# Kernel optimization log

Measured on AMD Instinct MI355X. Metric: run time of the kernel, lower is better.

## Reference

```python
import jax, jax.numpy as jnp
import numpy as np

NC = 80          # classes
REG_MAX = 16     # DFL bins
NK = 51          # 17*3 keypoint channels
KPT_SHAPE = (17, 3)
MAX_DET = 100
CONF_THRES = 0.25
STRIDES = (8, 16, 32)


def _conv1x1(f, w, b):
    # f: (B,C,H,W), w: (O,C), b: (O,) -> (B,O,H,W)
    return jnp.einsum('bchw,oc->bohw', f, w) + b[None, :, None, None]


def _make_anchors(shapes, strides, offset=0.5):
    pts, sts = [], []
    for (h, w), s in zip(shapes, strides):
        sx = jnp.arange(w, dtype=jnp.float32) + offset
        sy = jnp.arange(h, dtype=jnp.float32) + offset
        gy, gx = jnp.meshgrid(sy, sx, indexing='ij')
        pts.append(jnp.stack([gx, gy], -1).reshape(-1, 2))
        sts.append(jnp.full((h * w, 1), float(s), jnp.float32))
    # transposed as in _new_inference: anchors (2,A), strides (1,A)
    return jnp.concatenate(pts, 0).T, jnp.concatenate(sts, 0).T


def setup_inputs() -> dict:
    key = jax.random.key(0)
    ks = jax.random.split(key, 16)
    ch = (128, 256, 512)
    hw = ((80, 80), (40, 40), (20, 20))
    d = {}
    for i, (c, (h, w)) in enumerate(zip(ch, hw)):
        d[f'x{i}'] = jax.random.normal(ks[i], (16, c, h, w), jnp.float32)
    k = 3
    for name, oc in (('cv2', 4 * REG_MAX), ('cv3', NC), ('cv4', NK)):
        for i, c in enumerate(ch):
            d[f'{name}_w{i}'] = jax.random.normal(ks[k], (oc, c), jnp.float32) * 0.02
            d[f'{name}_b{i}'] = jnp.zeros((oc,), jnp.float32)
            k += 1
    return d


def reference(x0, x1, x2,
              cv2_w0, cv2_b0, cv2_w1, cv2_b1, cv2_w2, cv2_b2,
              cv3_w0, cv3_b0, cv3_w1, cv3_b1, cv3_w2, cv3_b2,
              cv4_w0, cv4_b0, cv4_w1, cv4_b1, cv4_w2, cv4_b2):
    feats = [x0, x1, x2]
    cv2 = [(cv2_w0, cv2_b0), (cv2_w1, cv2_b1), (cv2_w2, cv2_b2)]
    cv3 = [(cv3_w0, cv3_b0), (cv3_w1, cv3_b1), (cv3_w2, cv3_b2)]
    cv4 = [(cv4_w0, cv4_b0), (cv4_w1, cv4_b1), (cv4_w2, cv4_b2)]
    bs = x0.shape[0]

    # keypoint branch: cat over levels -> (bs, nk, A)
    kpt = jnp.concatenate(
        [_conv1x1(f, w, b).reshape(bs, NK, -1) for f, (w, b) in zip(feats, cv4)], -1)
    # box+cls branch -> (bs, 4*reg_max+nc, A)
    xcat = jnp.concatenate(
        [jnp.concatenate([_conv1x1(f, *cv2[i]), _conv1x1(f, *cv3[i])], 1).reshape(bs, 4 * REG_MAX + NC, -1)
         for i, f in enumerate(feats)], -1)
    box, cls = xcat[:, :4 * REG_MAX], xcat[:, 4 * REG_MAX:]

    shapes = [(f.shape[2], f.shape[3]) for f in feats]
    anchors, strides = _make_anchors(shapes, STRIDES)  # (2,A), (1,A)
    A = anchors.shape[1]

    # DFL decode: softmax over reg_max bins, expectation w/ arange weights
    p = jax.nn.softmax(box.reshape(bs, 4, REG_MAX, A), axis=2)
    dist = jnp.einsum('bfra,r->bfa', p, jnp.arange(REG_MAX, dtype=jnp.float32))
    lt, rb = dist[:, :2], dist[:, 2:]
    x1y1 = anchors[None] - lt
    x2y2 = anchors[None] + rb
    # xywh box coding, scaled by strides
    dbox = jnp.concatenate([(x1y1 + x2y2) * 0.5, x2y2 - x1y1], 1) * strides[None]  # (bs,4,A)

    # keypoint decode (Pose.kpts_decode, ndim==3)
    y = kpt.reshape(bs, KPT_SHAPE[0], KPT_SHAPE[1], A)
    kxy = (y[:, :, :2] * 2.0 + (anchors[None, None] - 0.5)) * strides[None, None]
    kv = jax.nn.sigmoid(y[:, :, 2:3])
    pred_kpts = jnp.concatenate([kxy, kv], 2).reshape(bs, NK, A).transpose(0, 2, 1)  # (bs,A,nk)

    # EfficientIdxNMS_TRT stand-in: sigmoid scores (score_activation=1),
    # class-agnostic deterministic top-k selection by best class score.
    scores = jax.nn.sigmoid(cls.transpose(0, 2, 1))  # (bs,A,nc)
    max_s = scores.max(-1)
    cls_id = jnp.argmax(scores, -1)
    top_s, top_i = jax.lax.top_k(max_s, MAX_DET)     # (bs,MAX_DET)
    num_dets = (top_s > CONF_THRES).sum(-1).astype(jnp.int32)[:, None]
    det_boxes = jnp.take_along_axis(dbox.transpose(0, 2, 1), top_i[..., None], 1)  # (bs,MAX_DET,4)
    det_classes = jnp.take_along_axis(cls_id, top_i, 1).astype(jnp.int32)
    # irregular keypoint gather via det indices (the pred_kpts[bs_indices, det_indices] step)
    det_kpts = jnp.take_along_axis(pred_kpts, top_i[..., None], 1).reshape(bs, MAX_DET, *KPT_SHAPE)
    return num_dets, det_boxes, top_s, det_classes, det_kpts
```

## Files before the change

kernel.cpp:

```cpp
#include <hip/hip_runtime.h>
#include <hip/hip_bf16.h>

#define NC 80
#define NK 51
#define REG_MAX 16
#define MAX_DET 100
#define A_TOT 8400
#define BS 16

#define OUT_NUM 0
#define OUT_BOX 16
#define OUT_SCORE (16 + 16*MAX_DET*4)
#define OUT_CLASS (OUT_SCORE + 16*MAX_DET)
#define OUT_KPT (OUT_CLASS + 16*MAX_DET)

static __device__ __forceinline__ unsigned long long mk_key(unsigned u, int a) {
    return ((unsigned long long)u << 32) | (unsigned)(0x7FFFFFFF - a);
}

__global__ __launch_bounds__(256) void scores_fused(
    const float* __restrict__ x0, const float* __restrict__ x1, const float* __restrict__ x2,
    const float* __restrict__ w0, const float* __restrict__ w1, const float* __restrict__ w2,
    const float* __restrict__ bias0, const float* __restrict__ bias1, const float* __restrict__ bias2,
    float* __restrict__ max_s,
    int* __restrict__ cls_id)
{
    __shared__ float fs[32 * 128];
    __shared__ float wsh[80 * 32];
    __shared__ float rm[4][128];
    __shared__ int   ri[4][128];

    int bid = blockIdx.x;
    const float *x, *w, *bias; int C, A, a_off, b, tile;
    if (bid < 64) {
        x = x2; w = w2; bias = bias2; C = 512; A = 400; a_off = 8000;
        b = bid >> 2; tile = bid & 3;
    } else if (bid < 272) {
        int r = bid - 64;
        x = x1; w = w1; bias = bias1; C = 256; A = 1600; a_off = 6400;
        b = r / 13; tile = r - b * 13;
    } else {
        int r = bid - 272;
        x = x0; w = w0; bias = bias0; C = 128; A = 6400; a_off = 0;
        b = r / 50; tile = r - b * 50;
    }
    int a0 = tile * 128;

    int t = threadIdx.x;
    int lane = t & 63;
    int wv = t >> 6;
    int oc0 = wv * 20;

    float acc0[20], acc1[20];
#pragma unroll
    for (int j = 0; j < 20; ++j) { float bv = bias[oc0 + j]; acc0[j] = bv; acc1[j] = bv; }

    const float* xb = x + (long)b * C * A;
    int nchunk = C >> 5;

    for (int kc = 0; kc < nchunk; ++kc) {
        __syncthreads();
#pragma unroll
        for (int i = 0; i < 4; ++i) {
            int idx = t + i * 256;
            int c = idx >> 5;
            int q = (idx & 31) * 4;
            int aa = a0 + q; if (aa > A - 4) aa = A - 4;
            float4 v = *(const float4*)(xb + (long)(kc * 32 + c) * A + aa);
            *(float4*)(&fs[c * 128 + q]) = v;
        }
#pragma unroll
        for (int i = 0; i < 3; ++i) {
            int idx = t + i * 256;
            if (idx < 640) {
                int oc = idx >> 3;
                int q = (idx & 7) * 4;
                float4 v = *(const float4*)(w + oc * C + kc * 32 + q);
                *(float4*)(&wsh[oc * 32 + q]) = v;
            }
        }
        __syncthreads();

#pragma unroll 1
        for (int c4 = 0; c4 < 32; c4 += 4) {
            float fa[4], fb[4];
#pragma unroll
            for (int cc = 0; cc < 4; ++cc) {
                fa[cc] = fs[(c4 + cc) * 128 + lane];
                fb[cc] = fs[(c4 + cc) * 128 + lane + 64];
            }
#pragma unroll
            for (int j = 0; j < 20; ++j) {
                float4 w4 = *(const float4*)(&wsh[(oc0 + j) * 32 + c4]);
                acc0[j] = fmaf(w4.x, fa[0], acc0[j]);
                acc0[j] = fmaf(w4.y, fa[1], acc0[j]);
                acc0[j] = fmaf(w4.z, fa[2], acc0[j]);
                acc0[j] = fmaf(w4.w, fa[3], acc0[j]);
                acc1[j] = fmaf(w4.x, fb[0], acc1[j]);
                acc1[j] = fmaf(w4.y, fb[1], acc1[j]);
                acc1[j] = fmaf(w4.z, fb[2], acc1[j]);
                acc1[j] = fmaf(w4.w, fb[3], acc1[j]);
            }
        }
    }

    float m0 = acc0[0], m1 = acc1[0]; int i0 = 0, i1 = 0;
#pragma unroll
    for (int j = 1; j < 20; ++j) {
        if (acc0[j] > m0) { m0 = acc0[j]; i0 = j; }
        if (acc1[j] > m1) { m1 = acc1[j]; i1 = j; }
    }
    i0 += oc0; i1 += oc0;

    rm[wv][lane] = m0;      ri[wv][lane] = i0;
    rm[wv][lane + 64] = m1; ri[wv][lane + 64] = i1;
    __syncthreads();
    if (wv == 0) {
#pragma unroll
        for (int p = 0; p < 2; ++p) {
            int a = lane + p * 64;
            float bm = rm[0][a]; int bi = ri[0][a];
#pragma unroll
            for (int v = 1; v < 4; ++v) {
                float om = rm[v][a];
                if (om > bm) { bm = om; bi = ri[v][a]; }
            }
            int ga = a0 + a;
            if (ga < A) {
                max_s[b * A_TOT + a_off + ga] = 1.0f / (1.0f + expf(-bm));
                cls_id[b * A_TOT + a_off + ga] = bi;
            }
        }
    }
}

__global__ __launch_bounds__(256) void topk_kernel(
    const float* __restrict__ max_s,
    const int* __restrict__ cls_id,
    float* __restrict__ out,
    int* __restrict__ top_idx)
{
    int b = blockIdx.x;
    int t = threadIdx.x;
    int lane = t & 63;
    int wv = t >> 6;

    __shared__ unsigned hist[4 * 256];
    __shared__ int tieIdx[A_TOT];
    __shared__ unsigned long long highKeys[128];
    __shared__ unsigned long long finalKeys[128];
    __shared__ int wmin[4];
    __shared__ unsigned s_prefix;
    __shared__ int s_k, s_nHigh, s_nTie, s_cnt, s_bcast;

    uint4 uu[9];
#pragma unroll
    for (int i = 0; i < 9; ++i) {
        int idx = t + i * 256;
        if (i < 8 || t < 52)
            uu[i] = *(const uint4*)((const unsigned*)(max_s + (long)b * A_TOT) + idx * 4);
        else
            uu[i] = make_uint4(0u, 0u, 0u, 0u);
    }

    if (t == 0) { s_prefix = 0; s_k = MAX_DET; s_nHigh = 0; s_nTie = 0; s_cnt = 0; }

    for (int pass = 0; pass < 4; ++pass) {
#pragma unroll
        for (int j = 0; j < 4; ++j) hist[t + j * 256] = 0;
        __syncthreads();

        unsigned pre = s_prefix;
        int k = s_k;
        int shHi = 32 - 8 * pass;
        int shD = 24 - 8 * pass;
#pragma unroll
        for (int i = 0; i < 9; ++i) {
            if (i < 8 || t < 52) {
                unsigned e[4] = { uu[i].x, uu[i].y, uu[i].z, uu[i].w };
#pragma unroll
                for (int j = 0; j < 4; ++j) {
                    bool cand = (pass == 0) ? true : ((e[j] >> shHi) == pre);
                    if (cand)
                        atomicAdd(&hist[(wv << 8) + ((e[j] >> shD) & 0xFF)], 1u);
                }
            }
        }
        __syncthreads();

        if (wv == 0) {
            unsigned c0 = 0, c1 = 0, c2 = 0, c3 = 0;
#pragma unroll
            for (int w = 0; w < 4; ++w) {
                const unsigned* hp = &hist[(w << 8) + lane * 4];
                c0 += hp[0]; c1 += hp[1]; c2 += hp[2]; c3 += hp[3];
            }
            unsigned s3 = c3, s2 = c2 + s3, s1 = c1 + s2, s0 = c0 + s1;
            unsigned tsum = s0;
#pragma unroll
            for (int off = 1; off < 64; off <<= 1) {
                unsigned o = __shfl_down(tsum, off, 64);
                if (lane + off < 64) tsum += o;
            }
            unsigned excl = tsum - s0;
            unsigned S0 = excl + s0, S1 = excl + s1, S2 = excl + s2, S3 = excl + s3;
            int ld = -1;
            unsigned uk = (unsigned)k;
            if (S3 >= uk)      ld = lane * 4 + 3;
            else if (S2 >= uk) ld = lane * 4 + 2;
            else if (S1 >= uk) ld = lane * 4 + 1;
            else if (S0 >= uk) ld = lane * 4 + 0;
            int d = ld;
#pragma unroll
            for (int off = 32; off > 0; off >>= 1) d = max(d, __shfl_xor(d, off, 64));
            int dn = d + 1;
            unsigned mine = 0;
            if (dn < 256 && lane == (dn >> 2)) {
                int e = dn & 3;
                mine = (e == 0) ? S0 : (e == 1) ? S1 : (e == 2) ? S2 : S3;
            }
#pragma unroll
            for (int off = 32; off > 0; off >>= 1) mine += __shfl_xor(mine, off, 64);
            if (lane == 0) {
                s_k = k - (int)mine;
                s_prefix = (pre << 8) | (unsigned)d;
            }
        }
        __syncthreads();
    }

    unsigned cut = s_prefix;
    int r = s_k;

#pragma unroll
    for (int i = 0; i < 9; ++i) {
        if (i < 8 || t < 52) {
            unsigned e[4] = { uu[i].x, uu[i].y, uu[i].z, uu[i].w };
#pragma unroll
            for (int j = 0; j < 4; ++j) {
                int a = (t + i * 256) * 4 + j;
                if (e[j] > cut) {
                    int p = atomicAdd(&s_nHigh, 1);
                    highKeys[p] = mk_key(e[j], a);
                } else if (e[j] == cut) {
                    int p = atomicAdd(&s_nTie, 1);
                    tieIdx[p] = a;
                }
            }
        }
    }
    __syncthreads();
    int m = s_nHigh;
    int nt = s_nTie;

    if (t < 128) finalKeys[t] = 0ull;
    __syncthreads();
    if (t < m) finalKeys[t] = highKeys[t];

    if (nt == r) {
        if (t < nt) finalKeys[m + t] = mk_key(cut, tieIdx[t]);
        __syncthreads();
    } else {
        __syncthreads();
        for (int j = 0; j < r; ++j) {
            int mn = 0x7FFFFFFF;
            for (int p = t; p < nt; p += 256) mn = min(mn, tieIdx[p]);
            for (int off = 32; off > 0; off >>= 1) mn = min(mn, __shfl_down(mn, off, 64));
            if (lane == 0) wmin[wv] = mn;
            __syncthreads();
            if (t == 0) {
                int v = min(min(wmin[0], wmin[1]), min(wmin[2], wmin[3]));
                s_bcast = v;
                finalKeys[m + j] = mk_key(cut, v);
            }
            __syncthreads();
            int v = s_bcast;
            for (int p = t; p < nt; p += 256)
                if (tieIdx[p] == v) tieIdx[p] = 0x7FFFFFFF;
            __syncthreads();
        }
    }

    for (int ksz = 2; ksz <= 128; ksz <<= 1) {
        for (int j = ksz >> 1; j > 0; j >>= 1) {
            if (t < 128) {
                int ixj = t ^ j;
                if (ixj > t) {
                    bool desc = ((t & ksz) == 0);
                    unsigned long long x = finalKeys[t], y = finalKeys[ixj];
                    bool sw = desc ? (x < y) : (x > y);
                    if (sw) { finalKeys[t] = y; finalKeys[ixj] = x; }
                }
            }
            __syncthreads();
        }
    }

    if (t < MAX_DET) {
        unsigned long long kk = finalKeys[t];
        float sc = __uint_as_float((unsigned)(kk >> 32));
        int a = 0x7FFFFFFF - (int)(kk & 0xFFFFFFFFull);
        out[OUT_SCORE + b * MAX_DET + t] = sc;
        out[OUT_CLASS + b * MAX_DET + t] = (float)cls_id[b * A_TOT + a];
        top_idx[b * MAX_DET + t] = a;
        if (sc > 0.25f) atomicAdd(&s_cnt, 1);
    }
    __syncthreads();
    if (t == 0) out[OUT_NUM + b] = (float)s_cnt;
}

__global__ __launch_bounds__(128) void decode_kernel(
    const float* __restrict__ x0, const float* __restrict__ x1, const float* __restrict__ x2,
    const float* __restrict__ w2_0, const float* __restrict__ b2_0,
    const float* __restrict__ w2_1, const float* __restrict__ b2_1,
    const float* __restrict__ w2_2, const float* __restrict__ b2_2,
    const float* __restrict__ w4_0, const float* __restrict__ b4_0,
    const float* __restrict__ w4_1, const float* __restrict__ b4_1,
    const float* __restrict__ w4_2, const float* __restrict__ b4_2,
    const int* __restrict__ top_idx,
    float* __restrict__ out)
{
    int b = blockIdx.y;
    int k = blockIdx.x;
    int a = top_idx[b * MAX_DET + k];

    const float* x; const float* w2; const float* bb2; const float* w4; const float* bb4;
    int C, A, W, a_local; float stride;
    if (a < 6400)      { x = x0; C = 128; A = 6400; W = 80; stride = 8.0f;  a_local = a;        w2 = w2_0; bb2 = b2_0; w4 = w4_0; bb4 = b4_0; }
    else if (a < 8000) { x = x1; C = 256; A = 1600; W = 40; stride = 16.0f; a_local = a - 6400; w2 = w2_1; bb2 = b2_1; w4 = w4_1; bb4 = b4_1; }
    else               { x = x2; C = 512; A = 400;  W = 20; stride = 32.0f; a_local = a - 8000; w2 = w2_2; bb2 = b2_2; w4 = w4_2; bb4 = b4_2; }

    __shared__ float fs[512];
    __shared__ float logits[64];
    __shared__ float kraw[NK];
    __shared__ float dist[4];

    int t = threadIdx.x;
    for (int c = t; c < C; c += 128)
        fs[c] = x[((long)b * C + c) * A + a_local];
    __syncthreads();

    if (t < 64 + NK) {
        const float* wrow; float acc;
        if (t < 64) { wrow = w2 + t * C; acc = bb2[t]; }
        else        { wrow = w4 + (t - 64) * C; acc = bb4[t - 64]; }
        for (int c = 0; c < C; c += 4) {
            float4 wv4 = *(const float4*)(wrow + c);
            float4 fv4 = *(const float4*)(&fs[c]);
            acc = fmaf(wv4.x, fv4.x, acc);
            acc = fmaf(wv4.y, fv4.y, acc);
            acc = fmaf(wv4.z, fv4.z, acc);
            acc = fmaf(wv4.w, fv4.w, acc);
        }
        if (t < 64) logits[t] = acc;
        else        kraw[t - 64] = acc;
    }
    __syncthreads();

    if (t < 4) {
        float mx = logits[t * 16];
#pragma unroll
        for (int r = 1; r < 16; ++r) mx = fmaxf(mx, logits[t * 16 + r]);
        float se = 0.0f, sw = 0.0f;
#pragma unroll
        for (int r = 0; r < 16; ++r) {
            float e = expf(logits[t * 16 + r] - mx);
            se += e; sw += e * (float)r;
        }
        dist[t] = sw / se;
    }
    __syncthreads();

    float ax = (float)(a_local % W) + 0.5f;
    float ay = (float)(a_local / W) + 0.5f;

    if (t == 0) {
        float x1c = ax - dist[0], y1c = ay - dist[1];
        float x2c = ax + dist[2], y2c = ay + dist[3];
        float* ob = out + OUT_BOX + ((long)b * MAX_DET + k) * 4;
        ob[0] = (x1c + x2c) * 0.5f * stride;
        ob[1] = (y1c + y2c) * 0.5f * stride;
        ob[2] = (x2c - x1c) * stride;
        ob[3] = (y2c - y1c) * stride;
    }
    if (t < 17) {
        float vx = kraw[t * 3], vy = kraw[t * 3 + 1], vv = kraw[t * 3 + 2];
        float gx = ax - 0.5f, gy = ay - 0.5f;
        float* ok = out + OUT_KPT + (((long)b * MAX_DET + k) * 17 + t) * 3;
        ok[0] = (vx * 2.0f + gx) * stride;
        ok[1] = (vy * 2.0f + gy) * stride;
        ok[2] = 1.0f / (1.0f + expf(-vv));
    }
}

extern "C" void kernel_launch(void* const* d_in, const int* in_sizes, int n_in,
                              void* d_out, int out_size, void* d_ws, size_t ws_size,
                              hipStream_t stream) {
    const float* x0 = (const float*)d_in[0];
    const float* x1 = (const float*)d_in[1];
    const float* x2 = (const float*)d_in[2];
    const float* w2[3] = {(const float*)d_in[3], (const float*)d_in[5], (const float*)d_in[7]};
    const float* b2[3] = {(const float*)d_in[4], (const float*)d_in[6], (const float*)d_in[8]};
    const float* w3[3] = {(const float*)d_in[9], (const float*)d_in[11], (const float*)d_in[13]};
    const float* b3[3] = {(const float*)d_in[10], (const float*)d_in[12], (const float*)d_in[14]};
    const float* w4[3] = {(const float*)d_in[15], (const float*)d_in[17], (const float*)d_in[19]};
    const float* b4[3] = {(const float*)d_in[16], (const float*)d_in[18], (const float*)d_in[20]};

    float* out = (float*)d_out;

    float* ws_maxs = (float*)d_ws;
    int* ws_cls = (int*)(ws_maxs + BS * A_TOT);
    int* ws_top = (int*)(ws_cls + BS * A_TOT);

    scores_fused<<<dim3(1072), 256, 0, stream>>>(
        x0, x1, x2, w3[0], w3[1], w3[2], b3[0], b3[1], b3[2], ws_maxs, ws_cls);
    topk_kernel<<<dim3(BS), 256, 0, stream>>>(ws_maxs, ws_cls, out, ws_top);
    decode_kernel<<<dim3(MAX_DET, BS), 128, 0, stream>>>(
        x0, x1, x2,
        w2[0], b2[0], w2[1], b2[1], w2[2], b2[2],
        w4[0], b4[0], w4[1], b4[1], w4[2], b4[2],
        ws_top, out);
}
```

Before: 300.4 us.

## Restructure class-score GEMM into register-tiled 512-anchor blocks with double-buffered weights

The fused class-score kernel is rebuilt as a templated tile routine. Each thread now computes 8 anchors by several output channels in registers, reading features straight from global memory with software prefetch instead of staging them in shared memory. Weights are double-buffered in padded shared memory, and the grid shrinks to 304 blocks of 512 threads. The 20x20 level is split over two blocks by output-channel halves, with a merge step added at the start of the top-k kernel. The aim is higher arithmetic intensity per load and fewer barriers, at the cost of heavier register pressure and fewer, larger blocks that may underfill the GPU.

```diff
diff --git a/kernel.cpp b/kernel.cpp
--- a/kernel.cpp
+++ b/kernel.cpp
@@ -18,125 +18,162 @@
     return ((unsigned long long)u << 32) | (unsigned)(0x7FFFFFFF - a);
 }
 
-__global__ __launch_bounds__(256) void scores_fused(
+template<int C, int A, int O>
+static __device__ __forceinline__ void score_tile(
+    const float* __restrict__ x, const float* __restrict__ w,
+    const float* __restrict__ bias,
+    int b, int a0, int oc_base,
+    float* __restrict__ out_m, int* __restrict__ out_i,
+    float* __restrict__ wsh, float* __restrict__ rm, int* __restrict__ ri)
+{
+    constexpr int NOC = 8 * O;
+    constexpr int NCH = C / 32;
+    constexpr int NF4 = NOC * 8;
+
+    int t = threadIdx.x;
+    int lane = t & 63;
+    int wv = t >> 6;
+    int ocw = oc_base + wv * O;
+
+    int aa = a0 + lane * 8;
+    if (aa > A - 8) aa = A - 8;
+    const float* xb = x + (long)b * C * A + aa;
+
+    float acc[O][8];
+#pragma unroll
+    for (int j = 0; j < O; ++j) {
+        float bv = bias[ocw + j];
+#pragma unroll
+        for (int q = 0; q < 8; ++q) acc[j][q] = bv;
+    }
+
+    bool st0 = (t < NF4), st1 = (t + 512 < NF4);
+    int o0 = t >> 3, q0 = t & 7;
+    int o1 = (t + 512) >> 3, q1 = (t + 512) & 7;
+
+    float4 s0, s1;
+    if (st0) s0 = *(const float4*)(w + (long)(oc_base + o0) * C + q0 * 4);
+    if (st1) s1 = *(const float4*)(w + (long)(oc_base + o1) * C + q1 * 4);
+
+    float4 fb[2][8];
+#pragma unroll
+    for (int cc = 0; cc < 4; ++cc) {
+        fb[0][cc * 2]     = *(const float4*)(xb + (long)cc * A);
+        fb[0][cc * 2 + 1] = *(const float4*)(xb + (long)cc * A + 4);
+    }
+    const float* fnext = xb + 4 * (long)A;
+
+    if (st0) *(float4*)&wsh[o0 * 36 + q0 * 4] = s0;
+    if (st1) *(float4*)&wsh[o1 * 36 + q1 * 4] = s1;
+    __syncthreads();
+
+    for (int kc = 0; kc < NCH; ++kc) {
+        int buf = kc & 1;
+        if (kc + 1 < NCH) {
+            const float* wn = w + (long)(kc + 1) * 32;
+            if (st0) s0 = *(const float4*)(wn + (long)(oc_base + o0) * C + q0 * 4);
+            if (st1) s1 = *(const float4*)(wn + (long)(oc_base + o1) * C + q1 * 4);
+        }
+        const float* wp = wsh + buf * (NOC * 36) + (wv * O) * 36;
+#pragma unroll
+        for (int c4 = 0; c4 < 8; ++c4) {
+            if (c4 < 7 || kc + 1 < NCH) {
+#pragma unroll
+                for (int cc = 0; cc < 4; ++cc) {
+                    fb[(c4 + 1) & 1][cc * 2]     = *(const float4*)(fnext + (long)cc * A);
+                    fb[(c4 + 1) & 1][cc * 2 + 1] = *(const float4*)(fnext + (long)cc * A + 4);
+                }
+                fnext += 4 * (long)A;
+            }
+            constexpr int DUMMY = 0; (void)DUMMY;
+            const int p = c4 & 1;
+#pragma unroll
+            for (int j = 0; j < O; ++j) {
+                float4 w4 = *(const float4*)(wp + j * 36 + c4 * 4);
+                float wc[4] = { w4.x, w4.y, w4.z, w4.w };
+#pragma unroll
+                for (int cc = 0; cc < 4; ++cc) {
+                    float4 fl = fb[p][cc * 2], fh = fb[p][cc * 2 + 1];
+                    acc[j][0] = fmaf(wc[cc], fl.x, acc[j][0]);
+                    acc[j][1] = fmaf(wc[cc], fl.y, acc[j][1]);
+                    acc[j][2] = fmaf(wc[cc], fl.z, acc[j][2]);
+                    acc[j][3] = fmaf(wc[cc], fl.w, acc[j][3]);
+                    acc[j][4] = fmaf(wc[cc], fh.x, acc[j][4]);
+                    acc[j][5] = fmaf(wc[cc], fh.y, acc[j][5]);
+                    acc[j][6] = fmaf(wc[cc], fh.z, acc[j][6]);
+                    acc[j][7] = fmaf(wc[cc], fh.w, acc[j][7]);
+                }
+            }
+        }
+        if (kc + 1 < NCH) {
+            float* wd = wsh + (buf ^ 1) * (NOC * 36);
+            if (st0) *(float4*)&wd[o0 * 36 + q0 * 4] = s0;
+            if (st1) *(float4*)&wd[o1 * 36 + q1 * 4] = s1;
+            __syncthreads();
+        }
+    }
+
+#pragma unroll
+    for (int q = 0; q < 8; ++q) {
+        float m = acc[0][q]; int mi = 0;
+#pragma unroll
+        for (int j = 1; j < O; ++j)
+            if (acc[j][q] > m) { m = acc[j][q]; mi = j; }
+        rm[wv * 512 + lane * 8 + q] = m;
+        ri[wv * 512 + lane * 8 + q] = ocw + mi;
+    }
+    __syncthreads();
+
+    {
+        float bm = rm[t]; int bi = ri[t];
+#pragma unroll
+        for (int v = 1; v < 8; ++v) {
+            float om = rm[v * 512 + t];
+            if (om > bm) { bm = om; bi = ri[v * 512 + t]; }
+        }
+        int ga = a0 + t;
+        if (ga < A) {
+            out_m[ga] = 1.0f / (1.0f + expf(-bm));
+            out_i[ga] = bi;
+        }
+    }
+}
+
+__global__ __launch_bounds__(512, 2) void scores_fused(
     const float* __restrict__ x0, const float* __restrict__ x1, const float* __restrict__ x2,
     const float* __restrict__ w0, const float* __restrict__ w1, const float* __restrict__ w2,
     const float* __restrict__ bias0, const float* __restrict__ bias1, const float* __restrict__ bias2,
     float* __restrict__ max_s,
-    int* __restrict__ cls_id)
+    int* __restrict__ cls_id,
+    float* __restrict__ l2m,
+    int* __restrict__ l2i)
 {
-    __shared__ float fs[32 * 128];
-    __shared__ float wsh[80 * 32];
-    __shared__ float rm[4][128];
-    __shared__ int   ri[4][128];
+    __shared__ float wsh[2 * 80 * 36];
+    __shared__ float rm[8 * 512];
+    __shared__ int   ri[8 * 512];
 
     int bid = blockIdx.x;
-    const float *x, *w, *bias; int C, A, a_off, b, tile;
     if (bid < 64) {
-        x = x2; w = w2; bias = bias2; C = 512; A = 400; a_off = 8000;
-        b = bid >> 2; tile = bid & 3;
-    } else if (bid < 272) {
+        int b = bid >> 2, tile = bid & 3;
+        score_tile<256, 1600, 10>(x1, w1, bias1, b, tile * 512, 0,
+            max_s + (long)b * A_TOT + 6400, cls_id + (long)b * A_TOT + 6400, wsh, rm, ri);
+    } else if (bid < 96) {
         int r = bid - 64;
-        x = x1; w = w1; bias = bias1; C = 256; A = 1600; a_off = 6400;
-        b = r / 13; tile = r - b * 13;
+        int b = r >> 1, h = r & 1;
+        score_tile<512, 400, 5>(x2, w2, bias2, b, 0, h * 40,
+            l2m + ((long)h * BS + b) * 400, l2i + ((long)h * BS + b) * 400, wsh, rm, ri);
     } else {
-        int r = bid - 272;
-        x = x0; w = w0; bias = bias0; C = 128; A = 6400; a_off = 0;
-        b = r / 50; tile = r - b * 50;
-    }
-    int a0 = tile * 128;
-
-    int t = threadIdx.x;
-    int lane = t & 63;
-    int wv = t >> 6;
-    int oc0 = wv * 20;
-
-    float acc0[20], acc1[20];
-#pragma unroll
-    for (int j = 0; j < 20; ++j) { float bv = bias[oc0 + j]; acc0[j] = bv; acc1[j] = bv; }
-
-    const float* xb = x + (long)b * C * A;
-    int nchunk = C >> 5;
-
-    for (int kc = 0; kc < nchunk; ++kc) {
-        __syncthreads();
-#pragma unroll
-        for (int i = 0; i < 4; ++i) {
-            int idx = t + i * 256;
-            int c = idx >> 5;
-            int q = (idx & 31) * 4;
-            int aa = a0 + q; if (aa > A - 4) aa = A - 4;
-            float4 v = *(const float4*)(xb + (long)(kc * 32 + c) * A + aa);
-            *(float4*)(&fs[c * 128 + q]) = v;
-        }
-#pragma unroll
-        for (int i = 0; i < 3; ++i) {
-            int idx = t + i * 256;
-            if (idx < 640) {
-                int oc = idx >> 3;
-                int q = (idx & 7) * 4;
-                float4 v = *(const float4*)(w + oc * C + kc * 32 + q);
-                *(float4*)(&wsh[oc * 32 + q]) = v;
-            }
-        }
-        __syncthreads();
-
-#pragma unroll 1
-        for (int c4 = 0; c4 < 32; c4 += 4) {
-            float fa[4], fb[4];
-#pragma unroll
-            for (int cc = 0; cc < 4; ++cc) {
-                fa[cc] = fs[(c4 + cc) * 128 + lane];
-                fb[cc] = fs[(c4 + cc) * 128 + lane + 64];
-            }
-#pragma unroll
-            for (int j = 0; j < 20; ++j) {
-                float4 w4 = *(const float4*)(&wsh[(oc0 + j) * 32 + c4]);
-                acc0[j] = fmaf(w4.x, fa[0], acc0[j]);
-                acc0[j] = fmaf(w4.y, fa[1], acc0[j]);
-                acc0[j] = fmaf(w4.z, fa[2], acc0[j]);
-                acc0[j] = fmaf(w4.w, fa[3], acc0[j]);
-                acc1[j] = fmaf(w4.x, fb[0], acc1[j]);
-                acc1[j] = fmaf(w4.y, fb[1], acc1[j]);
-                acc1[j] = fmaf(w4.z, fb[2], acc1[j]);
-                acc1[j] = fmaf(w4.w, fb[3], acc1[j]);
-            }
-        }
-    }
-
-    float m0 = acc0[0], m1 = acc1[0]; int i0 = 0, i1 = 0;
-#pragma unroll
-    for (int j = 1; j < 20; ++j) {
-        if (acc0[j] > m0) { m0 = acc0[j]; i0 = j; }
-        if (acc1[j] > m1) { m1 = acc1[j]; i1 = j; }
-    }
-    i0 += oc0; i1 += oc0;
-
-    rm[wv][lane] = m0;      ri[wv][lane] = i0;
-    rm[wv][lane + 64] = m1; ri[wv][lane + 64] = i1;
-    __syncthreads();
-    if (wv == 0) {
-#pragma unroll
-        for (int p = 0; p < 2; ++p) {
-            int a = lane + p * 64;
-            float bm = rm[0][a]; int bi = ri[0][a];
-#pragma unroll
-            for (int v = 1; v < 4; ++v) {
-                float om = rm[v][a];
-                if (om > bm) { bm = om; bi = ri[v][a]; }
-            }
-            int ga = a0 + a;
-            if (ga < A) {
-                max_s[b * A_TOT + a_off + ga] = 1.0f / (1.0f + expf(-bm));
-                cls_id[b * A_TOT + a_off + ga] = bi;
-            }
-        }
+        int r = bid - 96;
+        int b = r / 13, tile = r - b * 13;
+        score_tile<128, 6400, 10>(x0, w0, bias0, b, tile * 512, 0,
+            max_s + (long)b * A_TOT, cls_id + (long)b * A_TOT, wsh, rm, ri);
     }
 }
 
 __global__ __launch_bounds__(256) void topk_kernel(
-    const float* __restrict__ max_s,
-    const int* __restrict__ cls_id,
+    float* __restrict__ max_s,
+    int* __restrict__ cls_id,
+    const float* __restrict__ l2m, const int* __restrict__ l2i,
     float* __restrict__ out,
     int* __restrict__ top_idx)
 {
@@ -144,6 +181,17 @@
     int t = threadIdx.x;
     int lane = t & 63;
     int wv = t >> 6;
+
+    for (int a = t; a < 400; a += 256) {
+        float sA = l2m[(0 * BS + b) * 400 + a];
+        float sB = l2m[(1 * BS + b) * 400 + a];
+        int   iA = l2i[(0 * BS + b) * 400 + a];
+        int   iB = l2i[(1 * BS + b) * 400 + a];
+        bool ta = (sA >= sB);
+        max_s[(long)b * A_TOT + 8000 + a] = ta ? sA : sB;
+        cls_id[(long)b * A_TOT + 8000 + a] = ta ? iA : iB;
+    }
+    __syncthreads();
 
     __shared__ unsigned hist[4 * 256];
     __shared__ int tieIdx[A_TOT];
@@ -409,12 +457,15 @@
     float* out = (float*)d_out;
 
     float* ws_maxs = (float*)d_ws;
-    int* ws_cls = (int*)(ws_maxs + BS * A_TOT);
-    int* ws_top = (int*)(ws_cls + BS * A_TOT);
-
-    scores_fused<<<dim3(1072), 256, 0, stream>>>(
-        x0, x1, x2, w3[0], w3[1], w3[2], b3[0], b3[1], b3[2], ws_maxs, ws_cls);
-    topk_kernel<<<dim3(BS), 256, 0, stream>>>(ws_maxs, ws_cls, out, ws_top);
+    int*   ws_cls  = (int*)(ws_maxs + BS * A_TOT);
+    int*   ws_top  = (int*)(ws_cls + BS * A_TOT);
+    float* ws_l2m  = (float*)(ws_top + BS * MAX_DET);
+    int*   ws_l2i  = (int*)(ws_l2m + 2 * BS * 400);
+
+    scores_fused<<<dim3(304), 512, 0, stream>>>(
+        x0, x1, x2, w3[0], w3[1], w3[2], b3[0], b3[1], b3[2],
+        ws_maxs, ws_cls, ws_l2m, ws_l2i);
+    topk_kernel<<<dim3(BS), 256, 0, stream>>>(ws_maxs, ws_cls, ws_l2m, ws_l2i, out, ws_top);
     decode_kernel<<<dim3(MAX_DET, BS), 128, 0, stream>>>(
         x0, x1, x2,
         w2[0], b2[0], w2[1], b2[1], w2[2], b2[2],
```

Result: slower. 1.084 ms (+260.7%).
